# Kernel tuning notes

Hardware: AMD Instinct MI355X
Metric: run time of the kernel (lower is better)

## Reference

```python
import jax, jax.numpy as jnp
import numpy as np

NUM_HEADS = 12
AGENT_NUM = 49

def setup_inputs() -> dict:
    key = jax.random.key(0)
    ks = jax.random.split(key, 5)
    B, N, C = 32, 1176, 768
    x = jax.random.normal(ks[0], (B, N, C), dtype=jnp.float32)
    qkv_w = jax.random.normal(ks[1], (3 * C, C), dtype=jnp.float32) * 0.02
    qkv_b = jax.random.normal(ks[2], (3 * C,), dtype=jnp.float32) * 0.02
    proj_w = jax.random.normal(ks[3], (C, C), dtype=jnp.float32) * 0.02
    proj_b = jax.random.normal(ks[4], (C,), dtype=jnp.float32) * 0.02
    return {"x": x, "qkv_w": qkv_w, "qkv_b": qkv_b, "proj_w": proj_w,
            "proj_b": proj_b, "t_h": 14, "t_w": 14, "s_h": 28, "s_w": 28}

def _softmax_clamped(a):
    # original: float32 clamp to finfo min/max, then softmax(dim=-1)
    fi = jnp.finfo(jnp.float32)
    a = jnp.clip(a.astype(jnp.float32), fi.min, fi.max)
    return jax.nn.softmax(a, axis=-1)

def reference(x, qkv_w, qkv_b, proj_w, proj_b, t_h, t_w, s_h, s_w):
    B, N, C = x.shape
    H = NUM_HEADS
    hd = C // H
    scale = hd ** -0.5
    n_mt = 2 * t_h * t_w
    n_s = s_h * s_w

    qkv = (x @ qkv_w.T + qkv_b).reshape(B, N, 3, H, hd).transpose(2, 0, 3, 1, 4)
    q, k, v = qkv[0], qkv[1], qkv[2]  # [B,H,N,hd]

    q_mt, q_s = q[:, :, :n_mt], q[:, :, n_mt:]
    k_mt = k[:, :, :n_mt]
    v_mt = v[:, :, :n_mt]

    # stage 1: template/memory self-attention
    attn = _softmax_clamped(jnp.einsum('bhqd,bhkd->bhqk', q_mt, k_mt) * scale)
    x_mt = jnp.einsum('bhqk,bhkd->bhqd', attn, v_mt).transpose(0, 2, 1, 3).reshape(B, n_mt, C)

    # agent tokens: pool q_s (replicates original layout-scrambling reshape)
    p = int(AGENT_NUM ** 0.5)  # 7
    agent = q_s.reshape(B, s_h, s_w, C).transpose(0, 3, 1, 2)  # [B,C,s_h,s_w]
    agent = agent.reshape(B, C, p, s_h // p, p, s_w // p).mean(axis=(3, 5))  # exact AdaptiveAvgPool2d(7,7)
    agent = agent.reshape(B, C, AGENT_NUM).transpose(0, 2, 1)  # [B,agent_num,C]
    agent = agent.reshape(B, AGENT_NUM, H, hd).transpose(0, 2, 1, 3)  # [B,H,agent_num,hd]

    # stage 2: agent attends to all keys
    agent_attn = _softmax_clamped(jnp.einsum('bhad,bhkd->bhak', agent * scale, k))
    agent_v = jnp.einsum('bhak,bhkd->bhad', agent_attn, v)  # [B,H,agent_num,hd]

    # stage 3: search queries attend to agent tokens
    q_attn = _softmax_clamped(jnp.einsum('bhqd,bhad->bhqa', q_s * scale, agent))
    x_s = jnp.einsum('bhqa,bhad->bhqd', q_attn, agent_v).transpose(0, 2, 1, 3).reshape(B, n_s, C)

    out = jnp.concatenate([x_mt, x_s], axis=1)
    out = out @ proj_w.T + proj_b
    return out
```

## Files before the change

kernel.cpp:

```cpp
#include <hip/hip_runtime.h>

typedef __attribute__((ext_vector_type(8))) short short8;
typedef __attribute__((ext_vector_type(4))) short short4v;
typedef __attribute__((ext_vector_type(4))) float f32x4;
typedef unsigned short u16;

#define B_    32
#define N_    1176
#define C_    768
#define H_    12
#define HD_   64
#define NMT_  392
#define AG_   49
#define NEGBIG_ (-1.0e4f)

__device__ __forceinline__ u16 f2bf(float f) {
  unsigned u = __float_as_uint(f);
  unsigned r = (u + 0x7fffu + ((u >> 16) & 1u)) >> 16;
  return (u16)r;
}
__device__ __forceinline__ float bf2f(u16 s) {
  return __uint_as_float(((unsigned)s) << 16);
}

__device__ __forceinline__ int xcd_swz(int g, int nwg) {
  const int q = nwg >> 3, r = nwg & 7;
  const int xcd = g & 7, off = g >> 3;
  return (xcd < r ? xcd * (q + 1) : r * (q + 1) + (xcd - r) * q) + off;
}

template <int LO>
__global__ __launch_bounds__(256) void splitf(const float* __restrict__ in,
                                              u16* __restrict__ hi,
                                              u16* __restrict__ lo, int n4) {
  int i = blockIdx.x * 256 + threadIdx.x;
  const int stride = gridDim.x * 256;
  for (; i < n4; i += stride) {
    const float4 v = ((const float4*)in)[i];
    const float f[4] = {v.x, v.y, v.z, v.w};
    short4v h, l;
#pragma unroll
    for (int e = 0; e < 4; ++e) {
      u16 hb = f2bf(f[e]);
      h[e] = (short)hb;
      if (LO) l[e] = (short)f2bf(f[e] - bf2f(hb));
    }
    ((short4v*)hi)[i] = h;
    if (LO) ((short4v*)lo)[i] = l;
  }
}

__global__ __launch_bounds__(256, 3) void gemm_qkv(
    const u16* __restrict__ A, const u16* __restrict__ Bw,
    const float* __restrict__ bias, u16* __restrict__ qb, u16* __restrict__ kb,
    u16* __restrict__ vb, int Mch) {
  __shared__ u16 SH[17408];
  u16* As = SH;
  u16* Bs = SH + 8192;
  const int tid = threadIdx.x;
  const int swz = xcd_swz(blockIdx.x, gridDim.x);
  const int half = gridDim.x >> 1;
  const int cg = swz / half;
  const int rem = swz - cg * half;
  const int brow = rem / 9;
  const int bcol = cg * 9 + (rem - brow * 9);
  const int m0 = brow * 128, c0 = bcol * 128;
  const int lane = tid & 63, w = tid >> 6;
  const int wr = w >> 1, wc = w & 1;
  const int fr = lane & 15, ko = lane >> 4;
  const int lsw = (lane * 8) ^ (ko << 4);

  f32x4 acc[4][4];
#pragma unroll
  for (int m = 0; m < 4; ++m)
#pragma unroll
    for (int n = 0; n < 4; ++n) acc[m][n] = (f32x4)0.f;

  short8 ra[4], rb[4];
  auto LOADG = [&](int kt) {
#pragma unroll
    for (int i = 0; i < 4; ++i) {
      const int ch = tid + i * 256;
      const int row = ch >> 3, slotk = ch & 7;
      const int ar = min(m0 + row, Mch - 1);
      ra[i] = *(const short8*)&A[(size_t)ar * 768 + kt * 64 + slotk * 8];
      rb[i] = *(const short8*)&Bw[(size_t)(c0 + row) * 768 + kt * 64 + slotk * 8];
    }
  };
  auto WRITE = [&]() {
#pragma unroll
    for (int i = 0; i < 4; ++i) {
      const int ch = tid + i * 256;
      const int row = ch >> 3, slotk = ch & 7;
      const int s = slotk >> 2, sl = slotk & 3;
      const int off = (row >> 4) * 1024 + s * 512 +
                      ((sl * 128 + (row & 15) * 8) ^ (sl << 4));
      *(short8*)&As[off] = ra[i];
      *(short8*)&Bs[off] = rb[i];
    }
  };

  LOADG(0);
  for (int kt = 0; kt < 12; ++kt) {
    __syncthreads();
    WRITE();
    if (kt < 11) LOADG(kt + 1);
    __syncthreads();
#pragma unroll
    for (int s = 0; s < 2; ++s) {
      short8 af[4], bfr[4];
#pragma unroll
      for (int m = 0; m < 4; ++m)
        af[m] = *(const short8*)&As[((wr * 4 + m) * 2 + s) * 512 + lsw];
#pragma unroll
      for (int n = 0; n < 4; ++n)
        bfr[n] = *(const short8*)&Bs[((wc * 4 + n) * 2 + s) * 512 + lsw];
#pragma unroll
      for (int m = 0; m < 4; ++m)
#pragma unroll
        for (int n = 0; n < 4; ++n)
          acc[m][n] = __builtin_amdgcn_mfma_f32_16x16x32_bf16(af[m], bfr[n], acc[m][n], 0, 0, 0);
    }
  }

  __syncthreads();
  const int t = c0 / 768;
  const int hbase = (c0 % 768) >> 6;
  if (t < 2) {
#pragma unroll
    for (int n = 0; n < 4; ++n) {
      const int col = wc * 64 + n * 16 + fr;
      const float bv = bias[c0 + col];
#pragma unroll
      for (int m = 0; m < 4; ++m)
#pragma unroll
        for (int r = 0; r < 4; ++r) {
          const int row = wr * 64 + m * 16 + ko * 4 + r;
          SH[row * 136 + col] = f2bf(acc[m][n][r] + bv);
        }
    }
    __syncthreads();
    u16* dst = (t == 0) ? qb : kb;
    for (int it = tid; it < 2048; it += 256) {
      const int rt = it >> 4, half2 = (it >> 3) & 1, p = it & 7;
      const int mg = m0 + rt;
      if (mg < Mch) {
        const int bl = mg / N_, nt = mg - bl * N_;
        const short8 vv = *(const short8*)&SH[rt * 136 + half2 * 64 + p * 8];
        *(short8*)&dst[(((size_t)bl * H_ + hbase + half2) * N_ + nt) * 64 + p * 8] = vv;
      }
    }
  } else {
#pragma unroll
    for (int n = 0; n < 4; ++n) {
      const int col = wc * 64 + n * 16 + fr;
      const float bv = bias[c0 + col];
#pragma unroll
      for (int m = 0; m < 4; ++m)
#pragma unroll
        for (int r = 0; r < 4; ++r) {
          const int row = wr * 64 + m * 16 + ko * 4 + r;
          SH[col * 136 + row] = f2bf(acc[m][n][r] + bv);
        }
    }
    __syncthreads();
    for (int it = tid; it < 2048; it += 256) {
      const int ct = it >> 4, tc = it & 15;
      const int mg0 = m0 + tc * 8;
      if (mg0 < Mch) {
        const int bl = mg0 / N_, nt = mg0 - bl * N_;
        const int d = ct & 63, hh = hbase + (ct >> 6);
        const short8 vv = *(const short8*)&SH[ct * 136 + tc * 8];
        *(short8*)&vb[(((size_t)bl * H_ + hh) * 64 + d) * N_ + nt] = vv;
      }
    }
  }
}

__global__ __launch_bounds__(256, 3) void gemm_proj(
    const u16* __restrict__ Ahg, const u16* __restrict__ Bhg,
    const u16* __restrict__ Blg, const float* __restrict__ bias,
    float* __restrict__ out) {
  __shared__ u16 Ah[8192], Bh[8192], Bl[8192];
  const int tid = threadIdx.x;
  const int swz = xcd_swz(blockIdx.x, gridDim.x);
  const int brow = swz / 6, bcol = swz - brow * 6;
  const int m0 = brow * 128, c0 = bcol * 128;
  const int lane = tid & 63, w = tid >> 6;
  const int wr = w >> 1, wc = w & 1;
  const int fr = lane & 15, ko = lane >> 4;
  const int lsw = (lane * 8) ^ (ko << 4);

  f32x4 acc[4][4];
#pragma unroll
  for (int m = 0; m < 4; ++m)
#pragma unroll
    for (int n = 0; n < 4; ++n) acc[m][n] = (f32x4)0.f;

  short8 rah[4], rbh[4], rbl[4];
  auto LOADG = [&](int kt) {
#pragma unroll
    for (int i = 0; i < 4; ++i) {
      const int ch = tid + i * 256;
      const int row = ch >> 3, slotk = ch & 7;
      const size_t aoff = (size_t)(m0 + row) * 768 + kt * 64 + slotk * 8;
      const size_t boff = (size_t)(c0 + row) * 768 + kt * 64 + slotk * 8;
      rah[i] = *(const short8*)&Ahg[aoff];
      rbh[i] = *(const short8*)&Bhg[boff];
      rbl[i] = *(const short8*)&Blg[boff];
    }
  };
  auto WRITE = [&]() {
#pragma unroll
    for (int i = 0; i < 4; ++i) {
      const int ch = tid + i * 256;
      const int row = ch >> 3, slotk = ch & 7;
      const int s = slotk >> 2, sl = slotk & 3;
      const int off = (row >> 4) * 1024 + s * 512 +
                      ((sl * 128 + (row & 15) * 8) ^ (sl << 4));
      *(short8*)&Ah[off] = rah[i];
      *(short8*)&Bh[off] = rbh[i];
      *(short8*)&Bl[off] = rbl[i];
    }
  };

  LOADG(0);
  for (int kt = 0; kt < 12; ++kt) {
    __syncthreads();
    WRITE();
    if (kt < 11) LOADG(kt + 1);
    __syncthreads();
#pragma unroll
    for (int s = 0; s < 2; ++s) {
      short8 ah[4], bh[4], bl[4];
#pragma unroll
      for (int m = 0; m < 4; ++m)
        ah[m] = *(const short8*)&Ah[((wr * 4 + m) * 2 + s) * 512 + lsw];
#pragma unroll
      for (int n = 0; n < 4; ++n) {
        const int off = ((wc * 4 + n) * 2 + s) * 512 + lsw;
        bh[n] = *(const short8*)&Bh[off];
        bl[n] = *(const short8*)&Bl[off];
      }
#pragma unroll
      for (int m = 0; m < 4; ++m)
#pragma unroll
        for (int n = 0; n < 4; ++n) {
          acc[m][n] = __builtin_amdgcn_mfma_f32_16x16x32_bf16(ah[m], bh[n], acc[m][n], 0, 0, 0);
          acc[m][n] = __builtin_amdgcn_mfma_f32_16x16x32_bf16(ah[m], bl[n], acc[m][n], 0, 0, 0);
        }
    }
  }
#pragma unroll
  for (int n = 0; n < 4; ++n) {
    const int col = c0 + wc * 64 + n * 16 + fr;
    const float bv = bias[col];
#pragma unroll
    for (int m = 0; m < 4; ++m) {
      const int mg = m0 + wr * 64 + m * 16 + ko * 4;
#pragma unroll
      for (int r = 0; r < 4; ++r) out[(size_t)(mg + r) * 768 + col] = acc[m][n][r] + bv;
    }
  }
}

__global__ __launch_bounds__(256) void agent_pool(const u16* __restrict__ q,
                                                  u16* __restrict__ agent) {
  const int wid = threadIdx.x >> 6;
  const int lane = threadIdx.x & 63;
  const int row = blockIdx.x * 4 + wid;
  const int rem = row % (H_ * 64);
  const int b = row / (H_ * 64);
  const int h2 = rem / 64;
  const int a = rem % 64;
  if (a >= AG_) {
    agent[((size_t)b * H_ + h2) * 4096 + a * 64 + lane] = 0;
    return;
  }
  const int ap = a / 7, aq = a % 7;
  float s = 0.f;
#pragma unroll
  for (int i = 0; i < 4; ++i)
#pragma unroll
    for (int j = 0; j < 4; ++j) {
      const int g = (ap * 4 + i) * 336 + (aq * 4 + j) * 12 + h2;
      const int h = g / 784, n = g % 784;
      s += bf2f(q[(((size_t)b * H_ + h) * N_ + NMT_ + n) * HD_ + lane]);
    }
  agent[((size_t)b * H_ + h2) * 4096 + a * 64 + lane] = f2bf(s * 0.0625f);
}

__global__ __launch_bounds__(256, 3) void flash_attn(
    const u16* __restrict__ Q, int q_bh_str, int q_base, int q_row_max, int q_valid,
    const u16* __restrict__ K, int k_bh_str, int k_row_max,
    const u16* __restrict__ Vt, int vt_bh_str, int vt_pitch, int vt_col_max,
    int n_keys, int nkt,
    u16* __restrict__ cch, int b0,
    u16* __restrict__ avT, int mode) {
  __shared__ u16 Qs[4096], Ks[4096], Vts[4096], Ps[4096];
  __shared__ float Ss[64][65];
  __shared__ float mS[64], lS[64], aS[64];

  const int tid = threadIdx.x, bh = blockIdx.x;
  const int q0 = q_base + blockIdx.y * 56;
  const int lane = tid & 63, w = tid >> 6;
  const int fr = lane & 15, ko = lane >> 4;

  const u16* Qb = Q + (size_t)bh * q_bh_str;
  const u16* Kb = K + (size_t)bh * k_bh_str;
  const u16* Vb = Vt + (size_t)bh * vt_bh_str;

#pragma unroll
  for (int i = 0; i < 2; ++i) {
    const int ch = tid + i * 256;
    const int row = ch >> 3, c8 = (ch & 7) << 3;
    const int qr = min(q0 + row, q_row_max);
    const short8 v = *(const short8*)&Qb[(size_t)qr * 64 + c8];
    *(short8*)&Qs[(row * 64 + c8) ^ ((row & 7) << 3)] = v;
  }
  if (tid < 64) { mS[tid] = NEGBIG_; lS[tid] = 0.f; aS[tid] = 0.f; }

  f32x4 oacc[4];
#pragma unroll
  for (int d = 0; d < 4; ++d) oacc[d] = (f32x4)0.f;

  for (int kt = 0; kt < nkt; ++kt) {
#pragma unroll
    for (int i = 0; i < 2; ++i) {
      const int ch = tid + i * 256;
      const int row = ch >> 3, c8 = (ch & 7) << 3;
      const int kr = min(kt * 64 + row, k_row_max);
      const short8 v = *(const short8*)&Kb[(size_t)kr * 64 + c8];
      *(short8*)&Ks[(row * 64 + c8) ^ ((row & 7) << 3)] = v;
    }
#pragma unroll
    for (int i = 0; i < 2; ++i) {
      const int ch = tid + i * 256;
      const int row = ch >> 3, c8 = (ch & 7) << 3;
      const int col8 = kt * 64 + c8;
      const u16* src = &Vb[(size_t)row * vt_pitch];
      short8 v;
      if (col8 + 8 <= vt_col_max) {
        v = *(const short8*)&src[col8];
      } else {
#pragma unroll
        for (int e = 0; e < 8; ++e) v[e] = (short)src[min(col8 + e, vt_col_max - 1)];
      }
      *(short8*)&Vts[(row * 64 + c8) ^ ((row & 7) << 3)] = v;
    }
    __syncthreads();

    short8 aq[2];
#pragma unroll
    for (int s = 0; s < 2; ++s)
      aq[s] = *(const short8*)&Qs[((w * 16 + fr) * 64 + s * 32 + ko * 8) ^ ((fr & 7) << 3)];
#pragma unroll
    for (int j = 0; j < 4; ++j) {
      f32x4 sa = (f32x4)0.f;
#pragma unroll
      for (int s = 0; s < 2; ++s) {
        const short8 bk = *(const short8*)&Ks[((j * 16 + fr) * 64 + s * 32 + ko * 8) ^ ((fr & 7) << 3)];
        sa = __builtin_amdgcn_mfma_f32_16x16x32_bf16(aq[s], bk, sa, 0, 0, 0);
      }
      const int colg = kt * 64 + j * 16 + fr;
      const bool maskc = (colg >= n_keys);
#pragma unroll
      for (int r = 0; r < 4; ++r) {
        const int srow = w * 16 + ko * 4 + r;
        Ss[srow][j * 16 + fr] = maskc ? NEGBIG_ : sa[r] * 0.125f;
      }
    }
    __syncthreads();

    {
      const int r = tid >> 2, jj = tid & 3;
      float sv[16];
      float mx = NEGBIG_;
#pragma unroll
      for (int c = 0; c < 16; ++c) {
        sv[c] = Ss[r][jj * 16 + c];
        mx = fmaxf(mx, sv[c]);
      }
      mx = fmaxf(mx, __shfl_xor(mx, 1));
      mx = fmaxf(mx, __shfl_xor(mx, 2));
      const float mold = mS[r];
      const float mnew = fmaxf(mold, mx);
      float sum = 0.f;
#pragma unroll
      for (int c = 0; c < 16; ++c) {
        const bool mk = (kt * 64 + jj * 16 + c) >= n_keys;
        const float p = mk ? 0.f : __expf(sv[c] - mnew);
        sum += p;
        Ps[(r * 64 + jj * 16 + c) ^ ((r & 7) << 3)] = f2bf(p);
      }
      sum += __shfl_xor(sum, 1);
      sum += __shfl_xor(sum, 2);
      if (jj == 0) {
        const float alpha = __expf(mold - mnew);
        aS[r] = alpha;
        lS[r] = lS[r] * alpha + sum;
        mS[r] = mnew;
      }
    }
    __syncthreads();

    float al[4];
#pragma unroll
    for (int r = 0; r < 4; ++r) al[r] = aS[w * 16 + ko * 4 + r];
    short8 ap[2];
#pragma unroll
    for (int s = 0; s < 2; ++s)
      ap[s] = *(const short8*)&Ps[((w * 16 + fr) * 64 + s * 32 + ko * 8) ^ ((fr & 7) << 3)];
#pragma unroll
    for (int dj = 0; dj < 4; ++dj) {
      f32x4 o = oacc[dj];
#pragma unroll
      for (int r = 0; r < 4; ++r) o[r] *= al[r];
#pragma unroll
      for (int s = 0; s < 2; ++s) {
        const short8 bv = *(const short8*)&Vts[((dj * 16 + fr) * 64 + s * 32 + ko * 8) ^ ((fr & 7) << 3)];
        o = __builtin_amdgcn_mfma_f32_16x16x32_bf16(ap[s], bv, o, 0, 0, 0);
      }
      oacc[dj] = o;
    }
    __syncthreads();
  }

  float linv[4];
#pragma unroll
  for (int r = 0; r < 4; ++r) linv[r] = 1.f / fmaxf(lS[w * 16 + ko * 4 + r], 1e-30f);

  if (mode == 0) {
    const int b = bh / H_, h = bh % H_;
#pragma unroll
    for (int dj = 0; dj < 4; ++dj)
#pragma unroll
      for (int r = 0; r < 4; ++r) {
        const int rowl = w * 16 + ko * 4 + r;
        if (rowl < q_valid) {
          const size_t m = (size_t)(b0 + b) * N_ + q0 + rowl;
          cch[m * 768 + h * 64 + dj * 16 + fr] = f2bf(oacc[dj][r] * linv[r]);
        }
      }
  } else {
#pragma unroll
    for (int dj = 0; dj < 4; ++dj)
#pragma unroll
      for (int r = 0; r < 4; ++r) {
        const int a = w * 16 + ko * 4 + r;
        avT[(size_t)bh * 4096 + (dj * 16 + fr) * 64 + a] = f2bf(oacc[dj][r] * linv[r]);
      }
  }
}

extern "C" void kernel_launch(void* const* d_in, const int* in_sizes, int n_in,
                              void* d_out, int out_size, void* d_ws,
                              size_t ws_size, hipStream_t stream) {
  const float* x = (const float*)d_in[0];
  const float* qkv_w = (const float*)d_in[1];
  const float* qkv_b = (const float*)d_in[2];
  const float* proj_w = (const float*)d_in[3];
  const float* proj_b = (const float*)d_in[4];
  float* out = (float*)d_out;
  u16* ws = (u16*)d_ws;

  const size_t XBF = 28901376ull;
  const size_t QW = 2304ull * 768;
  const size_t PW = 768ull * 768;
  const size_t QKV1 = (size_t)H_ * N_ * HD_;
  const size_t AG1 = (size_t)H_ * 64 * 64;

  size_t o = 0;
  u16* xbf = ws + o; o += XBF;
  u16* qwh = ws + o; o += QW;
  u16* pwh = ws + o; o += PW;
  u16* pwl = ws + o; o += PW;
  u16* cch = ws + o; o += XBF;
  const size_t fixed_sh = o;
  const size_t per_sh = 3 * QKV1 + 2 * AG1;

  int cb = 1;
  const int cands[6] = {32, 16, 8, 4, 2, 1};
  for (int i = 0; i < 6; ++i)
    if ((fixed_sh + (size_t)cands[i] * per_sh) * 2 <= ws_size) { cb = cands[i]; break; }

  u16* qb = ws + o; o += cb * QKV1;
  u16* kb = ws + o; o += cb * QKV1;
  u16* vb = ws + o; o += cb * QKV1;
  u16* agent = ws + o; o += cb * AG1;
  u16* avT = ws + o; o += cb * AG1;

  splitf<0><<<2048, 256, 0, stream>>>(x, xbf, nullptr, (int)(XBF / 4));
  splitf<0><<<1024, 256, 0, stream>>>(qkv_w, qwh, nullptr, (int)(QW / 4));
  splitf<1><<<512, 256, 0, stream>>>(proj_w, pwh, pwl, (int)(PW / 4));

  const int nch = B_ / cb;
  for (int chn = 0; chn < nch; ++chn) {
    const int b0 = chn * cb;
    const int Mch = cb * N_;
    const int nrow = (Mch + 127) / 128;
    gemm_qkv<<<dim3(nrow * 18), 256, 0, stream>>>(
        xbf + (size_t)b0 * N_ * 768, qwh, qkv_b, qb, kb, vb, Mch);
    agent_pool<<<dim3(cb * 192), 256, 0, stream>>>(qb, agent);
    flash_attn<<<dim3(cb * H_, 1), 256, 0, stream>>>(
        agent, 4096, 0, 48, AG_, kb, N_ * HD_, N_ - 1,
        vb, N_ * HD_, N_, N_, N_, 19, nullptr, b0, avT, 1);
    flash_attn<<<dim3(cb * H_, 7), 256, 0, stream>>>(
        qb, N_ * HD_, 0, N_ - 1, 56, kb, N_ * HD_, N_ - 1,
        vb, N_ * HD_, N_, N_, NMT_, 7, cch, b0, nullptr, 0);
    flash_attn<<<dim3(cb * H_, 14), 256, 0, stream>>>(
        qb, N_ * HD_, NMT_, N_ - 1, 56, agent, 4096, 63,
        avT, 4096, 64, 64, AG_, 1, cch, b0, nullptr, 0);
  }
  gemm_proj<<<dim3(294 * 6), 256, 0, stream>>>(cch, pwh, pwl, proj_b, out);
}
```

Measured before the change: 534.5 us.

## Keep flash-attention softmax state in registers and drop shared score buffer

The flash attention kernel now does the online softmax directly on the MFMA accumulator registers. Row max and sum are reduced with lane shuffles instead of going through a shared-memory score matrix and per-row stats arrays, and Q is loaded straight into registers. Cutting shared memory allows the launch-bounds occupancy hint to rise from 3 to 5 blocks, and one __syncthreads per key tile is removed. In exchange there are more shuffle instructions, more register pressure under the tighter occupancy target, and a new XOR swizzle for the P tile that may cause bank conflicts.

After: 547.2 us. +2.4%, slower.

```diff
diff --git a/kernel.cpp b/kernel.cpp
--- a/kernel.cpp
+++ b/kernel.cpp
@@ -290,16 +290,14 @@
   agent[((size_t)b * H_ + h2) * 4096 + a * 64 + lane] = f2bf(s * 0.0625f);
 }
 
-__global__ __launch_bounds__(256, 3) void flash_attn(
+__global__ __launch_bounds__(256, 5) void flash_attn(
     const u16* __restrict__ Q, int q_bh_str, int q_base, int q_row_max, int q_valid,
     const u16* __restrict__ K, int k_bh_str, int k_row_max,
     const u16* __restrict__ Vt, int vt_bh_str, int vt_pitch, int vt_col_max,
     int n_keys, int nkt,
     u16* __restrict__ cch, int b0,
     u16* __restrict__ avT, int mode) {
-  __shared__ u16 Qs[4096], Ks[4096], Vts[4096], Ps[4096];
-  __shared__ float Ss[64][65];
-  __shared__ float mS[64], lS[64], aS[64];
+  __shared__ u16 Ks[4096], Vts[4096], Ps[4096];
 
   const int tid = threadIdx.x, bh = blockIdx.x;
   const int q0 = q_base + blockIdx.y * 56;
@@ -310,19 +308,23 @@
   const u16* Kb = K + (size_t)bh * k_bh_str;
   const u16* Vb = Vt + (size_t)bh * vt_bh_str;
 
-#pragma unroll
-  for (int i = 0; i < 2; ++i) {
-    const int ch = tid + i * 256;
-    const int row = ch >> 3, c8 = (ch & 7) << 3;
-    const int qr = min(q0 + row, q_row_max);
-    const short8 v = *(const short8*)&Qb[(size_t)qr * 64 + c8];
-    *(short8*)&Qs[(row * 64 + c8) ^ ((row & 7) << 3)] = v;
-  }
-  if (tid < 64) { mS[tid] = NEGBIG_; lS[tid] = 0.f; aS[tid] = 0.f; }
-
+  short8 aq[2];
+  {
+    const int qr = min(q0 + w * 16 + fr, q_row_max);
+#pragma unroll
+    for (int s = 0; s < 2; ++s)
+      aq[s] = *(const short8*)&Qb[(size_t)qr * 64 + s * 32 + ko * 8];
+  }
+
+  float m_[4], l_[4];
+#pragma unroll
+  for (int r = 0; r < 4; ++r) { m_[r] = NEGBIG_; l_[r] = 0.f; }
   f32x4 oacc[4];
 #pragma unroll
   for (int d = 0; d < 4; ++d) oacc[d] = (f32x4)0.f;
+
+  const int wpx = ko << 4;
+  const int rpx = ((fr >> 2) & 3) << 4;
 
   for (int kt = 0; kt < nkt; ++kt) {
 #pragma unroll
@@ -350,72 +352,64 @@
     }
     __syncthreads();
 
-    short8 aq[2];
-#pragma unroll
-    for (int s = 0; s < 2; ++s)
-      aq[s] = *(const short8*)&Qs[((w * 16 + fr) * 64 + s * 32 + ko * 8) ^ ((fr & 7) << 3)];
+    f32x4 sa[4];
 #pragma unroll
     for (int j = 0; j < 4; ++j) {
-      f32x4 sa = (f32x4)0.f;
+      sa[j] = (f32x4)0.f;
 #pragma unroll
       for (int s = 0; s < 2; ++s) {
         const short8 bk = *(const short8*)&Ks[((j * 16 + fr) * 64 + s * 32 + ko * 8) ^ ((fr & 7) << 3)];
-        sa = __builtin_amdgcn_mfma_f32_16x16x32_bf16(aq[s], bk, sa, 0, 0, 0);
-      }
-      const int colg = kt * 64 + j * 16 + fr;
-      const bool maskc = (colg >= n_keys);
-#pragma unroll
-      for (int r = 0; r < 4; ++r) {
-        const int srow = w * 16 + ko * 4 + r;
-        Ss[srow][j * 16 + fr] = maskc ? NEGBIG_ : sa[r] * 0.125f;
-      }
-    }
-    __syncthreads();
-
-    {
-      const int r = tid >> 2, jj = tid & 3;
-      float sv[16];
+        sa[j] = __builtin_amdgcn_mfma_f32_16x16x32_bf16(aq[s], bk, sa[j], 0, 0, 0);
+      }
+    }
+    bool mk[4];
+#pragma unroll
+    for (int j = 0; j < 4; ++j) mk[j] = (kt * 64 + j * 16 + fr) >= n_keys;
+
+#pragma unroll
+    for (int r = 0; r < 4; ++r) {
+      float v[4];
       float mx = NEGBIG_;
 #pragma unroll
-      for (int c = 0; c < 16; ++c) {
-        sv[c] = Ss[r][jj * 16 + c];
-        mx = fmaxf(mx, sv[c]);
+      for (int j = 0; j < 4; ++j) {
+        v[j] = mk[j] ? NEGBIG_ : sa[j][r] * 0.125f;
+        mx = fmaxf(mx, v[j]);
       }
       mx = fmaxf(mx, __shfl_xor(mx, 1));
       mx = fmaxf(mx, __shfl_xor(mx, 2));
-      const float mold = mS[r];
-      const float mnew = fmaxf(mold, mx);
+      mx = fmaxf(mx, __shfl_xor(mx, 4));
+      mx = fmaxf(mx, __shfl_xor(mx, 8));
+      const float mnew = fmaxf(m_[r], mx);
+      const float alpha = __expf(m_[r] - mnew);
       float sum = 0.f;
-#pragma unroll
-      for (int c = 0; c < 16; ++c) {
-        const bool mk = (kt * 64 + jj * 16 + c) >= n_keys;
-        const float p = mk ? 0.f : __expf(sv[c] - mnew);
+      u16 pb[4];
+#pragma unroll
+      for (int j = 0; j < 4; ++j) {
+        const float p = mk[j] ? 0.f : __expf(v[j] - mnew);
         sum += p;
-        Ps[(r * 64 + jj * 16 + c) ^ ((r & 7) << 3)] = f2bf(p);
+        pb[j] = f2bf(p);
       }
       sum += __shfl_xor(sum, 1);
       sum += __shfl_xor(sum, 2);
-      if (jj == 0) {
-        const float alpha = __expf(mold - mnew);
-        aS[r] = alpha;
-        lS[r] = lS[r] * alpha + sum;
-        mS[r] = mnew;
-      }
-    }
-    __syncthreads();
-
-    float al[4];
-#pragma unroll
-    for (int r = 0; r < 4; ++r) al[r] = aS[w * 16 + ko * 4 + r];
+      sum += __shfl_xor(sum, 4);
+      sum += __shfl_xor(sum, 8);
+      l_[r] = l_[r] * alpha + sum;
+      m_[r] = mnew;
+#pragma unroll
+      for (int dj = 0; dj < 4; ++dj) oacc[dj][r] *= alpha;
+      const int rowb = (w * 16 + ko * 4 + r) * 64;
+#pragma unroll
+      for (int j = 0; j < 4; ++j) Ps[(rowb + j * 16 + fr) ^ wpx] = pb[j];
+    }
+    __syncthreads();
+
     short8 ap[2];
 #pragma unroll
     for (int s = 0; s < 2; ++s)
-      ap[s] = *(const short8*)&Ps[((w * 16 + fr) * 64 + s * 32 + ko * 8) ^ ((fr & 7) << 3)];
+      ap[s] = *(const short8*)&Ps[((w * 16 + fr) * 64 + s * 32 + ko * 8) ^ rpx];
 #pragma unroll
     for (int dj = 0; dj < 4; ++dj) {
       f32x4 o = oacc[dj];
-#pragma unroll
-      for (int r = 0; r < 4; ++r) o[r] *= al[r];
 #pragma unroll
       for (int s = 0; s < 2; ++s) {
         const short8 bv = *(const short8*)&Vts[((dj * 16 + fr) * 64 + s * 32 + ko * 8) ^ ((fr & 7) << 3)];
@@ -428,7 +422,7 @@
 
   float linv[4];
 #pragma unroll
-  for (int r = 0; r < 4; ++r) linv[r] = 1.f / fmaxf(lS[w * 16 + ko * 4 + r], 1e-30f);
+  for (int r = 0; r < 4; ++r) linv[r] = 1.f / fmaxf(l_[r], 1e-30f);
 
   if (mode == 0) {
     const int b = bh / H_, h = bh % H_;
```
